# Performance work log

Measured on AMD Instinct MI355X. Metric: run time of the kernel, lower is better.

Reference implementation:

```python
import jax, jax.numpy as jnp
import numpy as np

B, S, R, H = 32, 512, 196, 1024


def setup_inputs() -> dict:
    key = jax.random.key(0)
    ks = jax.random.split(key, 12)
    sc = 1.0 / np.sqrt(H)
    return {
        "dns_feature": jax.random.normal(ks[0], (B, S, H), jnp.float32),
        "img_features": jax.random.normal(ks[1], (B, R, H), jnp.float32),
        # attention 1 params (dns_linear_1 has bias, img_linear_1 does not)
        "W_d1": jax.random.normal(ks[2], (H, H), jnp.float32) * sc,
        "b_d1": jax.random.normal(ks[3], (H,), jnp.float32) * sc,
        "W_i1": jax.random.normal(ks[4], (H, H), jnp.float32) * sc,
        "w_att1": jax.random.normal(ks[5], (2 * H,), jnp.float32) * sc,
        "b_att1": jax.random.normal(ks[6], (), jnp.float32) * sc,
        # attention 2 params (img_linear_2 has bias, dns_linear_2 does not)
        "W_d2": jax.random.normal(ks[7], (H, H), jnp.float32) * sc,
        "W_i2": jax.random.normal(ks[8], (H, H), jnp.float32) * sc,
        "b_i2": jax.random.normal(ks[9], (H,), jnp.float32) * sc,
        "w_att2": jax.random.normal(ks[10], (2 * H,), jnp.float32) * sc,
        "b_att2": jax.random.normal(ks[11], (), jnp.float32) * sc,
    }


def reference(dns_feature, img_features, W_d1, b_d1, W_i1, w_att1, b_att1,
              W_d2, W_i2, b_i2, w_att2, b_att2):
    h = dns_feature.shape[-1]
    # --- attention 1: dns attends over image regions ---
    # original: tanh(concat(Lin(dns_rep), Lin(img_rep))) -> att_linear_1.
    # tanh is elementwise and the concat linear is separable, so
    # score[b,s,r] = wA . tanh(W_d1 dns[b,s] + b_d1) + wB . tanh(W_i1 img[b,r]) + b_att1
    dns_p = jnp.tanh(jnp.einsum('bsh,oh->bso', dns_feature, W_d1) + b_d1)   # (B,S,H)
    img_p = jnp.tanh(jnp.einsum('brh,oh->bro', img_features, W_i1))          # (B,R,H)
    wA, wB = w_att1[:h], w_att1[h:]
    scores1 = (jnp.einsum('bsh,h->bs', dns_p, wA)[:, :, None]
               + jnp.einsum('brh,h->br', img_p, wB)[:, None, :] + b_att1)    # (B,S,R)
    visual_att = jax.nn.softmax(scores1, axis=-1)
    att_img_features = jnp.einsum('bsr,brh->bsh', visual_att, img_features)  # (B,S,H)
    # --- attention 2: attended image (per token i) attends over dns tokens j ---
    # concat order is [img_proj, dns_proj] here.
    img_p2 = jnp.tanh(jnp.einsum('bih,oh->bio', att_img_features, W_i2) + b_i2)  # (B,S,H)
    dns_p2 = jnp.tanh(jnp.einsum('bjh,oh->bjo', dns_feature, W_d2))              # (B,S,H)
    wI, wD = w_att2[:h], w_att2[h:]
    scores2 = (jnp.einsum('bih,h->bi', img_p2, wI)[:, :, None]
               + jnp.einsum('bjh,h->bj', dns_p2, wD)[:, None, :] + b_att2)       # (B,S,S)
    textual_att = jax.nn.softmax(scores2, axis=-1)
    att_dns_features = jnp.einsum('bij,bjh->bih', textual_att, dns_feature)      # (B,S,H)
    return att_dns_features, att_img_features
```

## Files before the change

kernel.cpp:

```cpp
#include <hip/hip_runtime.h>
#include <hip/hip_bf16.h>
#include <stdint.h>

typedef __bf16 bh;
typedef __bf16 bf16x8 __attribute__((ext_vector_type(8)));
typedef float f32x4 __attribute__((ext_vector_type(4)));
typedef unsigned int u32;

#define B_  32
#define S_  512
#define R_  196
#define H_  1024
#define BH  (B_ * H_)


__device__ __forceinline__ float fast_tanh(float x) {
  x = fminf(10.f, fmaxf(-10.f, x));
  float e = __expf(2.f * x);
  return (e - 1.f) / (e + 1.f);
}

__device__ __forceinline__ bf16x8 cvt8(const float4 a, const float4 b) {
  bf16x8 r;
  r[0] = (bh)a.x; r[1] = (bh)a.y; r[2] = (bh)a.z; r[3] = (bh)a.w;
  r[4] = (bh)b.x; r[5] = (bh)b.y; r[6] = (bh)b.z; r[7] = (bh)b.w;
  return r;
}

__device__ __forceinline__ void gload_lds16(const bh* g, bh* l) {
  __builtin_amdgcn_global_load_lds(
      (__attribute__((address_space(1))) void*)g,
      (__attribute__((address_space(3))) void*)l,
      16, 0, 0);
}

#define G_DNS 2097152
#define G_IMG 802816
#define G_W   131072
#define G_TOT (G_DNS + G_IMG + 2 * G_W)

__global__ __launch_bounds__(256)
void convert_kernel(const float* __restrict__ dns, const float* __restrict__ img,
                    const float* __restrict__ Wd2, const float* __restrict__ Wi1,
                    bh* __restrict__ dnsB, bh* __restrict__ imgB,
                    bh* __restrict__ wd2B, bh* __restrict__ wi1B) {
  for (int g = blockIdx.x * 256 + threadIdx.x; g < G_TOT; g += gridDim.x * 256) {
    const float* src; bh* dst; int off;
    if (g < G_DNS)                  { src = dns; dst = dnsB; off = g; }
    else if (g < G_DNS + G_IMG)     { src = img; dst = imgB; off = g - G_DNS; }
    else if (g < G_DNS + G_IMG + G_W) { src = Wd2; dst = wd2B; off = g - G_DNS - G_IMG; }
    else                            { src = Wi1; dst = wi1B; off = g - G_DNS - G_IMG - G_W; }
    float4 a = ((const float4*)src)[(size_t)off * 2];
    float4 b = ((const float4*)src)[(size_t)off * 2 + 1];
    ((bf16x8*)dst)[off] = cvt8(a, b);
  }
}


__global__ __launch_bounds__(256, 3)
void score_gemm_kernel(const bh* __restrict__ dnsB, const bh* __restrict__ imgB,
                       const bh* __restrict__ Wd2B, const bh* __restrict__ Wi1B,
                       const float* __restrict__ watt1, const float* __restrict__ watt2,
                       float* __restrict__ sPartD, float* __restrict__ sPartB) {
  __shared__ __align__(16) bh As[128 * 32];
  __shared__ __align__(16) bh Bs[128 * 32];
  __shared__ float sred[128];

  const int tid = threadIdx.x;
  const int wave = tid >> 6, lane = tid & 63;
  const int ny = blockIdx.x, my = blockIdx.y;

  const bh* X; const bh* W; const float* w; float* sp; int m0;
  if (my < 128) { X = dnsB; W = Wd2B; w = watt2 + H_; sp = sPartD; m0 = my * 128; }
  else          { X = imgB; W = Wi1B; w = watt1 + H_; sp = sPartB; m0 = (my - 128) * 128; }
  const int n0 = ny * 128;

  const int srow = wave * 32 + (lane >> 2);
  const int sseg = (lane & 3) * 8;
  const bh* Ag = X + ((size_t)(m0 + srow) * H_ + sseg);
  const bh* Bg = W + ((size_t)(n0 + srow) * H_ + sseg);
  bh* Al = As + (wave * 32) * 32;
  bh* Bl = Bs + (wave * 32) * 32;

  const int wm = wave >> 1, wn = wave & 1;
  const int col = lane & 15, quad = lane >> 4;

  f32x4 acc[4][4] = {};

  for (int kt = 0; kt < 32; ++kt) {
    if (kt) __syncthreads();
    const int ko = kt * 32;
    gload_lds16(Ag + ko,              Al);
    gload_lds16(Ag + ko + 16 * H_,    Al + 16 * 32);
    gload_lds16(Bg + ko,              Bl);
    gload_lds16(Bg + ko + 16 * H_,    Bl + 16 * 32);
    __syncthreads();

    bf16x8 af[4], bfr[4];
#pragma unroll
    for (int mi = 0; mi < 4; ++mi)
      af[mi] = *(const bf16x8*)(As + (wm * 64 + mi * 16 + col) * 32 + quad * 8);
#pragma unroll
    for (int ni = 0; ni < 4; ++ni)
      bfr[ni] = *(const bf16x8*)(Bs + (wn * 64 + ni * 16 + col) * 32 + quad * 8);

#pragma unroll
    for (int mi = 0; mi < 4; ++mi)
#pragma unroll
      for (int ni = 0; ni < 4; ++ni)
        acc[mi][ni] = __builtin_amdgcn_mfma_f32_16x16x32_bf16(af[mi], bfr[ni], acc[mi][ni], 0, 0, 0);
  }

  float wv[4];
#pragma unroll
  for (int ni = 0; ni < 4; ++ni) wv[ni] = w[n0 + wn * 64 + ni * 16 + col];

  float ppv[4][4];
#pragma unroll
  for (int mi = 0; mi < 4; ++mi) {
#pragma unroll
    for (int reg = 0; reg < 4; ++reg) {
      float pp = 0.f;
#pragma unroll
      for (int ni = 0; ni < 4; ++ni) pp += fast_tanh(acc[mi][ni][reg]) * wv[ni];
      pp += __shfl_xor(pp, 1);
      pp += __shfl_xor(pp, 2);
      pp += __shfl_xor(pp, 4);
      pp += __shfl_xor(pp, 8);
      ppv[mi][reg] = pp;
    }
  }

  if (wn == 0 && col == 0) {
#pragma unroll
    for (int mi = 0; mi < 4; ++mi)
#pragma unroll
      for (int reg = 0; reg < 4; ++reg)
        sred[wm * 64 + mi * 16 + quad * 4 + reg] = ppv[mi][reg];
  }
  __syncthreads();
  if (wn == 1 && col == 0) {
#pragma unroll
    for (int mi = 0; mi < 4; ++mi)
#pragma unroll
      for (int reg = 0; reg < 4; ++reg) {
        int ml = wm * 64 + mi * 16 + quad * 4 + reg;
        sp[(size_t)(m0 + ml) * 8 + ny] = sred[ml] + ppv[mi][reg];
      }
  }
}

__global__ __launch_bounds__(512)
void softmax_kernel(const float* __restrict__ sPartD, const float* __restrict__ sPartB,
                    float* __restrict__ q, float* __restrict__ p) {
  __shared__ float red[8];
  const int b = blockIdx.x, tid = threadIdx.x;
  const int wave = tid >> 6, lane = tid & 63;

  {
    const float4* p4 = (const float4*)(sPartD + (size_t)(b * S_ + tid) * 8);
    float4 x0 = p4[0], x1 = p4[1];
    float x = x0.x + x0.y + x0.z + x0.w + x1.x + x1.y + x1.z + x1.w;
    float wm = x;
#pragma unroll
    for (int msk = 32; msk; msk >>= 1) wm = fmaxf(wm, __shfl_xor(wm, msk));
    if (!lane) red[wave] = wm;
    __syncthreads();
    float bm = red[0];
#pragma unroll
    for (int i = 1; i < 8; ++i) bm = fmaxf(bm, red[i]);
    __syncthreads();
    float e = __expf(x - bm);
    float ws = e;
#pragma unroll
    for (int msk = 32; msk; msk >>= 1) ws += __shfl_xor(ws, msk);
    if (!lane) red[wave] = ws;
    __syncthreads();
    float bs = 0.f;
#pragma unroll
    for (int i = 0; i < 8; ++i) bs += red[i];
    q[b * S_ + tid] = e / bs;
    __syncthreads();
  }
  {
    float x = -3.0e38f;
    if (tid < R_) {
      const float4* p4 = (const float4*)(sPartB + (size_t)(b * R_ + tid) * 8);
      float4 x0 = p4[0], x1 = p4[1];
      x = x0.x + x0.y + x0.z + x0.w + x1.x + x1.y + x1.z + x1.w;
    }
    float wm = x;
#pragma unroll
    for (int msk = 32; msk; msk >>= 1) wm = fmaxf(wm, __shfl_xor(wm, msk));
    if (!lane) red[wave] = wm;
    __syncthreads();
    float bm = red[0];
#pragma unroll
    for (int i = 1; i < 8; ++i) bm = fmaxf(bm, red[i]);
    __syncthreads();
    float e = (tid < R_) ? __expf(x - bm) : 0.f;
    float ws = e;
#pragma unroll
    for (int msk = 32; msk; msk >>= 1) ws += __shfl_xor(ws, msk);
    if (!lane) red[wave] = ws;
    __syncthreads();
    float bs = 0.f;
#pragma unroll
    for (int i = 0; i < 8; ++i) bs += red[i];
    if (tid < R_) p[b * R_ + tid] = e / bs;
  }
}

__global__ __launch_bounds__(256)
void wsum_kernel(const float* __restrict__ dns, const float* __restrict__ img,
                 const float* __restrict__ q, const float* __restrict__ p,
                 float* __restrict__ uPart, float* __restrict__ vPart) {
  __shared__ float qs[64];
  const int b = blockIdx.x, tid = threadIdx.x, zc = blockIdx.y;
  const int h = tid * 4;
  float4 a = {0.f, 0.f, 0.f, 0.f};
  if (zc < 16) {
    const int j0 = zc * 32;
    if (tid < 32) qs[tid] = q[b * S_ + j0 + tid];
    __syncthreads();
    const float* Xb = dns + ((size_t)(b * S_ + j0) * H_ + h);
#pragma unroll
    for (int jj = 0; jj < 32; ++jj) {
      float4 xv = *(const float4*)(Xb + (size_t)jj * H_);
      float qv = qs[jj];
      a.x += qv * xv.x; a.y += qv * xv.y; a.z += qv * xv.z; a.w += qv * xv.w;
    }
    *(float4*)(uPart + (size_t)zc * BH + (size_t)b * H_ + h) = a;
  } else {
    const int j0 = (zc - 16) * 49;
    if (tid < 49) qs[tid] = p[b * R_ + j0 + tid];
    __syncthreads();
    const float* Xb = img + ((size_t)(b * R_ + j0) * H_ + h);
#pragma unroll
    for (int jj = 0; jj < 49; ++jj) {
      float4 xv = *(const float4*)(Xb + (size_t)jj * H_);
      float qv = qs[jj];
      a.x += qv * xv.x; a.y += qv * xv.y; a.z += qv * xv.z; a.w += qv * xv.w;
    }
    *(float4*)(vPart + (size_t)(zc - 16) * BH + (size_t)b * H_ + h) = a;
  }
}

__global__ __launch_bounds__(256)
void combine_kernel(const float* __restrict__ uPart, const float* __restrict__ vPart,
                    float* __restrict__ u, float* __restrict__ v) {
  const int b = blockIdx.x, tid = threadIdx.x;
  const int i = b * 256 + tid;
  float4 a = {0.f, 0.f, 0.f, 0.f};
#pragma unroll
  for (int c = 0; c < 16; ++c) {
    float4 s = ((const float4*)(uPart + (size_t)c * BH))[i];
    a.x += s.x; a.y += s.y; a.z += s.z; a.w += s.w;
  }
  ((float4*)u)[i] = a;
  float4 cacc = {0.f, 0.f, 0.f, 0.f};
#pragma unroll
  for (int c = 0; c < 4; ++c) {
    float4 s = ((const float4*)(vPart + (size_t)c * BH))[i];
    cacc.x += s.x; cacc.y += s.y; cacc.z += s.z; cacc.w += s.w;
  }
  ((float4*)v)[i] = cacc;
}

__global__ __launch_bounds__(256)
void bcast_kernel(const float* __restrict__ u, const float* __restrict__ v,
                  float* __restrict__ out) {
  const int PER4 = B_ * S_ * H_ / 4;
  const int t = blockIdx.x * 256 + threadIdx.x;
  const int which = (t >= PER4);
  const int r = t - which * PER4;
  const int b = r >> 17;
  const int h4 = r & 255;
  const float4 val = ((const float4*)((which ? v : u) + (size_t)b * H_))[h4];
  ((float4*)out)[t] = val;
}


extern "C" void kernel_launch(void* const* d_in, const int* in_sizes, int n_in,
                              void* d_out, int out_size, void* d_ws, size_t ws_size,
                              hipStream_t stream) {
  const float* dns   = (const float*)d_in[0];
  const float* img   = (const float*)d_in[1];
  const float* Wi1   = (const float*)d_in[4];
  const float* watt1 = (const float*)d_in[5];
  const float* Wd2   = (const float*)d_in[7];
  const float* watt2 = (const float*)d_in[10];
  float* out = (float*)d_out;

  float* ws = (float*)d_ws;
  float* sPartD = ws;
  float* sPartB = ws + 131072;
  float* q      = ws + 181248;
  float* p      = ws + 197632;
  float* uPart  = ws + 203904;
  float* vPart  = ws + 728192;
  float* u      = ws + 859264;
  float* v      = ws + 892032;
  bh* dnsB = (bh*)(ws + 924800);
  bh* imgB = (bh*)(ws + 9313408);
  bh* wd2B = (bh*)(ws + 12524672);
  bh* wi1B = (bh*)(ws + 13048960);

  convert_kernel<<<2048, 256, 0, stream>>>(dns, img, Wd2, Wi1, dnsB, imgB, wd2B, wi1B);
  score_gemm_kernel<<<dim3(8, 128 + 49), 256, 0, stream>>>(
      dnsB, imgB, wd2B, wi1B, watt1, watt2, sPartD, sPartB);
  softmax_kernel<<<B_, 512, 0, stream>>>(sPartD, sPartB, q, p);
  wsum_kernel<<<dim3(B_, 20), 256, 0, stream>>>(dns, img, q, p, uPart, vPart);
  combine_kernel<<<B_, 256, 0, stream>>>(uPart, vPart, u, v);
  bcast_kernel<<<32768, 256, 0, stream>>>(u, v, out);
}
```

Measured before the change: 330.9 us.

## Double-buffer score GEMM, swizzle LDS, remap blocks, fuse softmax and combine kernels

The score GEMM now double-buffers its LDS tiles so the next K-slice load overlaps the MFMAs. It XOR-swizzles the LDS column segments to reduce bank conflicts and remaps the flat block index so blocks sharing a weight tile run close together. The softmax is folded into the weighted-sum kernel, with each block recomputing the full row softmax, and the partial-sum combine is folded into a broadcast kernel that writes 32 rows per block. This cuts two launches and the q/p/u/v round trips, at the price of redundant softmax work and fewer, longer-running blocks in the broadcast.

After: 323.9 us. 2.1% less time.

```diff
diff --git a/kernel.cpp b/kernel.cpp
--- a/kernel.cpp
+++ b/kernel.cpp
@@ -5,7 +5,6 @@
 typedef __bf16 bh;
 typedef __bf16 bf16x8 __attribute__((ext_vector_type(8)));
 typedef float f32x4 __attribute__((ext_vector_type(4)));
-typedef unsigned int u32;
 
 #define B_  32
 #define S_  512
@@ -46,10 +45,10 @@
                     bh* __restrict__ wd2B, bh* __restrict__ wi1B) {
   for (int g = blockIdx.x * 256 + threadIdx.x; g < G_TOT; g += gridDim.x * 256) {
     const float* src; bh* dst; int off;
-    if (g < G_DNS)                  { src = dns; dst = dnsB; off = g; }
-    else if (g < G_DNS + G_IMG)     { src = img; dst = imgB; off = g - G_DNS; }
+    if (g < G_DNS)                    { src = dns; dst = dnsB; off = g; }
+    else if (g < G_DNS + G_IMG)       { src = img; dst = imgB; off = g - G_DNS; }
     else if (g < G_DNS + G_IMG + G_W) { src = Wd2; dst = wd2B; off = g - G_DNS - G_IMG; }
-    else                            { src = Wi1; dst = wi1B; off = g - G_DNS - G_IMG - G_W; }
+    else                              { src = Wi1; dst = wi1B; off = g - G_DNS - G_IMG - G_W; }
     float4 a = ((const float4*)src)[(size_t)off * 2];
     float4 b = ((const float4*)src)[(size_t)off * 2 + 1];
     ((bf16x8*)dst)[off] = cvt8(a, b);
@@ -62,53 +61,67 @@
                        const bh* __restrict__ Wd2B, const bh* __restrict__ Wi1B,
                        const float* __restrict__ watt1, const float* __restrict__ watt2,
                        float* __restrict__ sPartD, float* __restrict__ sPartB) {
-  __shared__ __align__(16) bh As[128 * 32];
-  __shared__ __align__(16) bh Bs[128 * 32];
+  __shared__ __align__(16) bh As[2][128 * 32];
+  __shared__ __align__(16) bh Bs[2][128 * 32];
   __shared__ float sred[128];
 
   const int tid = threadIdx.x;
   const int wave = tid >> 6, lane = tid & 63;
-  const int ny = blockIdx.x, my = blockIdx.y;
+
+  const int d = blockIdx.x;
+  const int k = (d & 7) * 177 + (d >> 3);
+  const int my = k >> 3, ny = k & 7;
 
   const bh* X; const bh* W; const float* w; float* sp; int m0;
   if (my < 128) { X = dnsB; W = Wd2B; w = watt2 + H_; sp = sPartD; m0 = my * 128; }
   else          { X = imgB; W = Wi1B; w = watt1 + H_; sp = sPartB; m0 = (my - 128) * 128; }
   const int n0 = ny * 128;
 
-  const int srow = wave * 32 + (lane >> 2);
-  const int sseg = (lane & 3) * 8;
-  const bh* Ag = X + ((size_t)(m0 + srow) * H_ + sseg);
-  const bh* Bg = W + ((size_t)(n0 + srow) * H_ + sseg);
-  bh* Al = As + (wave * 32) * 32;
-  bh* Bl = Bs + (wave * 32) * 32;
+  const int srow  = wave * 32 + (lane >> 2);
+  const int ssege = (((lane & 3) ^ ((lane >> 2) & 2)) * 8);
+  const bh* Ag = X + ((size_t)(m0 + srow) * H_ + ssege);
+  const bh* Bg = W + ((size_t)(n0 + srow) * H_ + ssege);
+  const int lw = wave * 32 * 32;
 
   const int wm = wave >> 1, wn = wave & 1;
   const int col = lane & 15, quad = lane >> 4;
+  const int qx8 = ((quad ^ (col & 2)) * 8);
 
   f32x4 acc[4][4] = {};
 
+  {
+    gload_lds16(Ag,            &As[0][lw]);
+    gload_lds16(Ag + 16 * H_,  &As[0][lw + 16 * 32]);
+    gload_lds16(Bg,            &Bs[0][lw]);
+    gload_lds16(Bg + 16 * H_,  &Bs[0][lw + 16 * 32]);
+  }
+  __syncthreads();
+
   for (int kt = 0; kt < 32; ++kt) {
-    if (kt) __syncthreads();
-    const int ko = kt * 32;
-    gload_lds16(Ag + ko,              Al);
-    gload_lds16(Ag + ko + 16 * H_,    Al + 16 * 32);
-    gload_lds16(Bg + ko,              Bl);
-    gload_lds16(Bg + ko + 16 * H_,    Bl + 16 * 32);
-    __syncthreads();
+    const int cur = kt & 1;
+    if (kt + 1 < 32) {
+      const int ko = (kt + 1) * 32;
+      gload_lds16(Ag + ko,            &As[cur ^ 1][lw]);
+      gload_lds16(Ag + ko + 16 * H_,  &As[cur ^ 1][lw + 16 * 32]);
+      gload_lds16(Bg + ko,            &Bs[cur ^ 1][lw]);
+      gload_lds16(Bg + ko + 16 * H_,  &Bs[cur ^ 1][lw + 16 * 32]);
+    }
 
     bf16x8 af[4], bfr[4];
 #pragma unroll
     for (int mi = 0; mi < 4; ++mi)
-      af[mi] = *(const bf16x8*)(As + (wm * 64 + mi * 16 + col) * 32 + quad * 8);
+      af[mi] = *(const bf16x8*)(&As[cur][(wm * 64 + mi * 16 + col) * 32 + qx8]);
 #pragma unroll
     for (int ni = 0; ni < 4; ++ni)
-      bfr[ni] = *(const bf16x8*)(Bs + (wn * 64 + ni * 16 + col) * 32 + quad * 8);
+      bfr[ni] = *(const bf16x8*)(&Bs[cur][(wn * 64 + ni * 16 + col) * 32 + qx8]);
 
 #pragma unroll
     for (int mi = 0; mi < 4; ++mi)
 #pragma unroll
       for (int ni = 0; ni < 4; ++ni)
         acc[mi][ni] = __builtin_amdgcn_mfma_f32_16x16x32_bf16(af[mi], bfr[ni], acc[mi][ni], 0, 0, 0);
+
+    __syncthreads();
   }
 
   float wv[4];
@@ -150,96 +163,78 @@
   }
 }
 
-__global__ __launch_bounds__(512)
-void softmax_kernel(const float* __restrict__ sPartD, const float* __restrict__ sPartB,
-                    float* __restrict__ q, float* __restrict__ p) {
-  __shared__ float red[8];
-  const int b = blockIdx.x, tid = threadIdx.x;
+__global__ __launch_bounds__(256)
+void wsum_kernel(const float* __restrict__ dns, const float* __restrict__ img,
+                 const float* __restrict__ sPartD, const float* __restrict__ sPartB,
+                 float* __restrict__ uPart, float* __restrict__ vPart) {
+  __shared__ float red[4];
+  __shared__ float es[512];
+  const int b = blockIdx.x, tid = threadIdx.x, zc = blockIdx.y;
   const int wave = tid >> 6, lane = tid & 63;
-
-  {
-    const float4* p4 = (const float4*)(sPartD + (size_t)(b * S_ + tid) * 8);
-    float4 x0 = p4[0], x1 = p4[1];
-    float x = x0.x + x0.y + x0.z + x0.w + x1.x + x1.y + x1.z + x1.w;
-    float wm = x;
-#pragma unroll
-    for (int msk = 32; msk; msk >>= 1) wm = fmaxf(wm, __shfl_xor(wm, msk));
-    if (!lane) red[wave] = wm;
-    __syncthreads();
-    float bm = red[0];
-#pragma unroll
-    for (int i = 1; i < 8; ++i) bm = fmaxf(bm, red[i]);
-    __syncthreads();
-    float e = __expf(x - bm);
-    float ws = e;
-#pragma unroll
-    for (int msk = 32; msk; msk >>= 1) ws += __shfl_xor(ws, msk);
-    if (!lane) red[wave] = ws;
-    __syncthreads();
-    float bs = 0.f;
-#pragma unroll
-    for (int i = 0; i < 8; ++i) bs += red[i];
-    q[b * S_ + tid] = e / bs;
-    __syncthreads();
-  }
-  {
+  const int h = tid * 4;
+
+  if (zc < 16) {
+    const float4* p4 = (const float4*)(sPartD + (size_t)b * S_ * 8);
+    float4 a0 = p4[tid * 2],        a1 = p4[tid * 2 + 1];
+    float4 c0 = p4[(tid + 256) * 2], c1 = p4[(tid + 256) * 2 + 1];
+    float x0 = a0.x + a0.y + a0.z + a0.w + a1.x + a1.y + a1.z + a1.w;
+    float x1 = c0.x + c0.y + c0.z + c0.w + c1.x + c1.y + c1.z + c1.w;
+    float m = fmaxf(x0, x1);
+#pragma unroll
+    for (int msk = 32; msk; msk >>= 1) m = fmaxf(m, __shfl_xor(m, msk));
+    if (!lane) red[wave] = m;
+    __syncthreads();
+    float bm = fmaxf(fmaxf(red[0], red[1]), fmaxf(red[2], red[3]));
+    __syncthreads();
+    float e0 = __expf(x0 - bm), e1 = __expf(x1 - bm);
+    es[tid] = e0; es[tid + 256] = e1;
+    float s = e0 + e1;
+#pragma unroll
+    for (int msk = 32; msk; msk >>= 1) s += __shfl_xor(s, msk);
+    if (!lane) red[wave] = s;
+    __syncthreads();
+    const float inv = 1.f / (red[0] + red[1] + red[2] + red[3]);
+
+    const int j0 = zc * 32;
+    const float* Xb = dns + ((size_t)(b * S_ + j0) * H_ + h);
+    float4 a = {0.f, 0.f, 0.f, 0.f};
+#pragma unroll
+    for (int jj = 0; jj < 32; ++jj) {
+      float4 xv = *(const float4*)(Xb + (size_t)jj * H_);
+      float qv = es[j0 + jj] * inv;
+      a.x += qv * xv.x; a.y += qv * xv.y; a.z += qv * xv.z; a.w += qv * xv.w;
+    }
+    *(float4*)(uPart + (size_t)zc * BH + (size_t)b * H_ + h) = a;
+  } else {
+    const float4* p4 = (const float4*)(sPartB + (size_t)b * R_ * 8);
     float x = -3.0e38f;
     if (tid < R_) {
-      const float4* p4 = (const float4*)(sPartB + (size_t)(b * R_ + tid) * 8);
-      float4 x0 = p4[0], x1 = p4[1];
-      x = x0.x + x0.y + x0.z + x0.w + x1.x + x1.y + x1.z + x1.w;
-    }
-    float wm = x;
-#pragma unroll
-    for (int msk = 32; msk; msk >>= 1) wm = fmaxf(wm, __shfl_xor(wm, msk));
-    if (!lane) red[wave] = wm;
-    __syncthreads();
-    float bm = red[0];
-#pragma unroll
-    for (int i = 1; i < 8; ++i) bm = fmaxf(bm, red[i]);
+      float4 a0 = p4[tid * 2], a1 = p4[tid * 2 + 1];
+      x = a0.x + a0.y + a0.z + a0.w + a1.x + a1.y + a1.z + a1.w;
+    }
+    float m = x;
+#pragma unroll
+    for (int msk = 32; msk; msk >>= 1) m = fmaxf(m, __shfl_xor(m, msk));
+    if (!lane) red[wave] = m;
+    __syncthreads();
+    float bm = fmaxf(fmaxf(red[0], red[1]), fmaxf(red[2], red[3]));
     __syncthreads();
     float e = (tid < R_) ? __expf(x - bm) : 0.f;
-    float ws = e;
-#pragma unroll
-    for (int msk = 32; msk; msk >>= 1) ws += __shfl_xor(ws, msk);
-    if (!lane) red[wave] = ws;
-    __syncthreads();
-    float bs = 0.f;
-#pragma unroll
-    for (int i = 0; i < 8; ++i) bs += red[i];
-    if (tid < R_) p[b * R_ + tid] = e / bs;
-  }
-}
-
-__global__ __launch_bounds__(256)
-void wsum_kernel(const float* __restrict__ dns, const float* __restrict__ img,
-                 const float* __restrict__ q, const float* __restrict__ p,
-                 float* __restrict__ uPart, float* __restrict__ vPart) {
-  __shared__ float qs[64];
-  const int b = blockIdx.x, tid = threadIdx.x, zc = blockIdx.y;
-  const int h = tid * 4;
-  float4 a = {0.f, 0.f, 0.f, 0.f};
-  if (zc < 16) {
-    const int j0 = zc * 32;
-    if (tid < 32) qs[tid] = q[b * S_ + j0 + tid];
-    __syncthreads();
-    const float* Xb = dns + ((size_t)(b * S_ + j0) * H_ + h);
-#pragma unroll
-    for (int jj = 0; jj < 32; ++jj) {
-      float4 xv = *(const float4*)(Xb + (size_t)jj * H_);
-      float qv = qs[jj];
-      a.x += qv * xv.x; a.y += qv * xv.y; a.z += qv * xv.z; a.w += qv * xv.w;
-    }
-    *(float4*)(uPart + (size_t)zc * BH + (size_t)b * H_ + h) = a;
-  } else {
+    es[tid] = e;
+    float s = e;
+#pragma unroll
+    for (int msk = 32; msk; msk >>= 1) s += __shfl_xor(s, msk);
+    if (!lane) red[wave] = s;
+    __syncthreads();
+    const float inv = 1.f / (red[0] + red[1] + red[2] + red[3]);
+
     const int j0 = (zc - 16) * 49;
-    if (tid < 49) qs[tid] = p[b * R_ + j0 + tid];
-    __syncthreads();
     const float* Xb = img + ((size_t)(b * R_ + j0) * H_ + h);
+    float4 a = {0.f, 0.f, 0.f, 0.f};
 #pragma unroll
     for (int jj = 0; jj < 49; ++jj) {
       float4 xv = *(const float4*)(Xb + (size_t)jj * H_);
-      float qv = qs[jj];
+      float qv = es[j0 + jj] * inv;
       a.x += qv * xv.x; a.y += qv * xv.y; a.z += qv * xv.z; a.w += qv * xv.w;
     }
     *(float4*)(vPart + (size_t)(zc - 16) * BH + (size_t)b * H_ + h) = a;
@@ -247,37 +242,30 @@
 }
 
 __global__ __launch_bounds__(256)
-void combine_kernel(const float* __restrict__ uPart, const float* __restrict__ vPart,
-                    float* __restrict__ u, float* __restrict__ v) {
-  const int b = blockIdx.x, tid = threadIdx.x;
-  const int i = b * 256 + tid;
-  float4 a = {0.f, 0.f, 0.f, 0.f};
+void bcast_kernel(const float* __restrict__ uPart, const float* __restrict__ vPart,
+                  float* __restrict__ out) {
+  const int id = blockIdx.x;
+  const int b = id >> 4, sc = id & 15;
+  const int t = threadIdx.x;
+
+  float4 u4 = {0.f, 0.f, 0.f, 0.f};
 #pragma unroll
   for (int c = 0; c < 16; ++c) {
-    float4 s = ((const float4*)(uPart + (size_t)c * BH))[i];
-    a.x += s.x; a.y += s.y; a.z += s.z; a.w += s.w;
-  }
-  ((float4*)u)[i] = a;
-  float4 cacc = {0.f, 0.f, 0.f, 0.f};
+    float4 s = ((const float4*)(uPart + (size_t)c * BH + (size_t)b * H_))[t];
+    u4.x += s.x; u4.y += s.y; u4.z += s.z; u4.w += s.w;
+  }
+  float4 v4 = {0.f, 0.f, 0.f, 0.f};
 #pragma unroll
   for (int c = 0; c < 4; ++c) {
-    float4 s = ((const float4*)(vPart + (size_t)c * BH))[i];
-    cacc.x += s.x; cacc.y += s.y; cacc.z += s.z; cacc.w += s.w;
-  }
-  ((float4*)v)[i] = cacc;
-}
-
-__global__ __launch_bounds__(256)
-void bcast_kernel(const float* __restrict__ u, const float* __restrict__ v,
-                  float* __restrict__ out) {
+    float4 s = ((const float4*)(vPart + (size_t)c * BH + (size_t)b * H_))[t];
+    v4.x += s.x; v4.y += s.y; v4.z += s.z; v4.w += s.w;
+  }
+
   const int PER4 = B_ * S_ * H_ / 4;
-  const int t = blockIdx.x * 256 + threadIdx.x;
-  const int which = (t >= PER4);
-  const int r = t - which * PER4;
-  const int b = r >> 17;
-  const int h4 = r & 255;
-  const float4 val = ((const float4*)((which ? v : u) + (size_t)b * H_))[h4];
-  ((float4*)out)[t] = val;
+  float4* o0 = (float4*)out + ((size_t)(b * S_ + sc * 32)) * 256 + t;
+  float4* o1 = o0 + PER4;
+#pragma unroll
+  for (int s = 0; s < 32; ++s) { o0[(size_t)s * 256] = u4; o1[(size_t)s * 256] = v4; }
 }
 
 
@@ -295,22 +283,16 @@
   float* ws = (float*)d_ws;
   float* sPartD = ws;
   float* sPartB = ws + 131072;
-  float* q      = ws + 181248;
-  float* p      = ws + 197632;
-  float* uPart  = ws + 203904;
-  float* vPart  = ws + 728192;
-  float* u      = ws + 859264;
-  float* v      = ws + 892032;
-  bh* dnsB = (bh*)(ws + 924800);
-  bh* imgB = (bh*)(ws + 9313408);
-  bh* wd2B = (bh*)(ws + 12524672);
-  bh* wi1B = (bh*)(ws + 13048960);
+  float* uPart  = ws + 181248;
+  float* vPart  = ws + 705536;
+  bh* dnsB = (bh*)(ws + 836608);
+  bh* imgB = (bh*)(ws + 9225216);
+  bh* wd2B = (bh*)(ws + 12436480);
+  bh* wi1B = (bh*)(ws + 12960768);
 
   convert_kernel<<<2048, 256, 0, stream>>>(dns, img, Wd2, Wi1, dnsB, imgB, wd2B, wi1B);
-  score_gemm_kernel<<<dim3(8, 128 + 49), 256, 0, stream>>>(
+  score_gemm_kernel<<<1416, 256, 0, stream>>>(
       dnsB, imgB, wd2B, wi1B, watt1, watt2, sPartD, sPartB);
-  softmax_kernel<<<B_, 512, 0, stream>>>(sPartD, sPartB, q, p);
-  wsum_kernel<<<dim3(B_, 20), 256, 0, stream>>>(dns, img, q, p, uPart, vPart);
-  combine_kernel<<<B_, 256, 0, stream>>>(uPart, vPart, u, v);
-  bcast_kernel<<<32768, 256, 0, stream>>>(u, v, out);
-}
+  wsum_kernel<<<dim3(B_, 20), 256, 0, stream>>>(dns, img, sPartD, sPartB, uPart, vPart);
+  bcast_kernel<<<512, 256, 0, stream>>>(uPart, vPart, out);
+}
```
